# Kernel tuning notes

Hardware: AMD Instinct MI355X
Metric: run time of the kernel (lower is better)

## Reference

```python
import jax, jax.numpy as jnp
import numpy as np


def _procrustes_align(X, Y):
    """Batched similarity-transform (scipy-style Procrustes, reflection allowed).
    Aligns Y (pred) to X (target). X, Y: [B, N, 3]. Returns aligned Y: [B, N, 3].
    """
    muX = X.mean(axis=1, keepdims=True)                      # [B,1,3]
    muY = Y.mean(axis=1, keepdims=True)
    X0 = X - muX
    Y0 = Y - muY
    normX = jnp.sqrt((X0 ** 2).sum(axis=(1, 2), keepdims=True))  # [B,1,1]
    normY = jnp.sqrt((Y0 ** 2).sum(axis=(1, 2), keepdims=True))
    X0n = X0 / normX
    Y0n = Y0 / normY
    # 3x3 cross-covariance per batch element
    M = jnp.einsum('bni,bnj->bij', X0n, Y0n)                 # [B,3,3]
    U, s, Vt = jnp.linalg.svd(M)                             # batched tiny SVD
    # Optimal rotation Q = V @ U^T = (U @ Vt)^T  (minimizes ||Y0n @ Q - X0n||)
    Q = jnp.swapaxes(jnp.matmul(U, Vt), -1, -2)              # [B,3,3]
    traceTA = s.sum(-1)[:, None, None]                       # [B,1,1]
    Z = normX * traceTA * jnp.einsum('bni,bij->bnj', Y0n, Q) + muX
    return Z


def setup_inputs() -> dict:
    key = jax.random.key(0)
    k1, k2 = jax.random.split(key)
    B, N = 262144, 21
    pred_kp3d = jax.random.normal(k1, (B, N, 3), dtype=jnp.float32)
    target_kp3d = jax.random.normal(k2, (B, N, 3), dtype=jnp.float32)
    return {"pred_kp3d": pred_kp3d, "target_kp3d": target_kp3d}


def reference(pred_kp3d, target_kp3d):
    pred_aligned = _procrustes_align(target_kp3d, pred_kp3d)
    # mean per-joint Euclidean distance (PA-MPJPE style)
    err = jnp.sqrt(((pred_aligned - target_kp3d) ** 2).sum(-1)).mean()
    return err
```

## Files before the change

### kernel.cpp

```cpp
#include <hip/hip_runtime.h>
#include <math.h>

#define NPTS 21
#define FLB  63
#define BPW  32
#define THREADS 64
#define TVEC (BPW * FLB / 4)
#define FULLR (TVEC / 64)
#define TAILL (TVEC % 64)
#define KMAX 11

__device__ __forceinline__ void async_cp16(const float* g, float* l) {
    __builtin_amdgcn_global_load_lds(
        (__attribute__((address_space(1))) void*)g,
        (__attribute__((address_space(3))) void*)l,
        16, 0, 0);
}

__global__ __launch_bounds__(THREADS, 3)
void pa_mpjpe(const float* __restrict__ pred,
              const float* __restrict__ targ,
              float* __restrict__ ws,
              int B)
{
    __shared__ __align__(16) float ly[BPW * FLB];
    __shared__ __align__(16) float lx[BPW * FLB];

    const int lane = threadIdx.x & 63;
    const int b    = lane & (BPW - 1);
    const int sub  = (lane >> 5) & 1;
    const int b0   = blockIdx.x * BPW;

    {
        const float* gp = pred + (size_t)b0 * FLB;
        const float* gt = targ + (size_t)b0 * FLB;
        #pragma unroll
        for (int j = 0; j < FULLR; ++j)
            async_cp16(gp + 4 * (j * 64 + lane), ly + 4 * (j * 64));
        if (lane < TAILL)
            async_cp16(gp + 4 * (FULLR * 64 + lane), ly + 4 * (FULLR * 64));
        #pragma unroll
        for (int j = 0; j < FULLR; ++j)
            async_cp16(gt + 4 * (j * 64 + lane), lx + 4 * (j * 64));
        if (lane < TAILL)
            async_cp16(gt + 4 * (FULLR * 64 + lane), lx + 4 * (FULLR * 64));
    }
    __builtin_amdgcn_s_waitcnt(0x0F70);

    float py0[KMAX], py1[KMAX], py2[KMAX];
    float sy0=0.f, sy1=0.f, sy2=0.f, syy=0.f;
    float sx0=0.f, sx1=0.f, sx2=0.f;
    float m00=0,m01=0,m02=0, m10=0,m11=0,m12=0, m20=0,m21=0,m22=0;
    const int base = b * FLB;
    #pragma unroll
    for (int k = 0; k < KMAX; ++k) {
        const int n = 2 * k + sub;
        if (n < NPTS) {
            const int o = base + 3 * n;
            float a = ly[o+0], e = ly[o+1], c = ly[o+2];
            float u = lx[o+0], v = lx[o+1], x2 = lx[o+2];
            py0[k] = a; py1[k] = e; py2[k] = c;
            sy0 += a; sy1 += e; sy2 += c;
            syy = fmaf(a, a, fmaf(e, e, fmaf(c, c, syy)));
            sx0 += u; sx1 += v; sx2 += x2;
            m00 = fmaf(u,a,m00); m01 = fmaf(u,e,m01); m02 = fmaf(u,c,m02);
            m10 = fmaf(v,a,m10); m11 = fmaf(v,e,m11); m12 = fmaf(v,c,m12);
            m20 = fmaf(x2,a,m20); m21 = fmaf(x2,e,m21); m22 = fmaf(x2,c,m22);
        } else {
            py0[k] = 0.f; py1[k] = 0.f; py2[k] = 0.f;
        }
    }

    #define COMB(v) { v += __shfl_xor(v, 32, 64); }
    COMB(sy0) COMB(sy1) COMB(sy2) COMB(syy)
    COMB(sx0) COMB(sx1) COMB(sx2)
    COMB(m00) COMB(m01) COMB(m02)
    COMB(m10) COMB(m11) COMB(m12)
    COMB(m20) COMB(m21) COMB(m22)
    #undef COMB

    const float invN = 1.0f / (float)NPTS;
    float mux0 = sx0*invN, mux1 = sx1*invN, mux2 = sx2*invN;
    float muy0 = sy0*invN, muy1 = sy1*invN, muy2 = sy2*invN;
    float ny2  = syy - (sy0*sy0 + sy1*sy1 + sy2*sy2) * invN;
    float c00 = m00 - sx0*sy0*invN, c01 = m01 - sx0*sy1*invN, c02 = m02 - sx0*sy2*invN;
    float c10 = m10 - sx1*sy0*invN, c11 = m11 - sx1*sy1*invN, c12 = m12 - sx1*sy2*invN;
    float c20 = m20 - sx2*sy0*invN, c21 = m21 - sx2*sy1*invN, c22 = m22 - sx2*sy2*invN;

    float q00=c00, q01=c10, q02=c20,
          q10=c01, q11=c11, q12=c21,
          q20=c02, q21=c12, q22=c22;
    #pragma unroll
    for (int it = 0; it < 6; ++it) {
        float C00 = q11*q22 - q12*q21;
        float C01 = q12*q20 - q10*q22;
        float C02 = q10*q21 - q11*q20;
        float C10 = q02*q21 - q01*q22;
        float C11 = q00*q22 - q02*q20;
        float C12 = q01*q20 - q00*q21;
        float C20 = q01*q12 - q02*q11;
        float C21 = q02*q10 - q00*q12;
        float C22 = q00*q11 - q01*q10;
        float det = q00*C00 + q01*C01 + q02*C02;
        float ad  = fmaxf(fabsf(det), 1e-30f);
        float sdet = copysignf(ad, det);
        float g  = __expf(0.333333333f * __logf(ad));
        float ha = 0.5f / g;
        float hb = 0.5f * g / sdet;
        q00 = ha*q00 + hb*C00; q01 = ha*q01 + hb*C01; q02 = ha*q02 + hb*C02;
        q10 = ha*q10 + hb*C10; q11 = ha*q11 + hb*C11; q12 = ha*q12 + hb*C12;
        q20 = ha*q20 + hb*C20; q21 = ha*q21 + hb*C21; q22 = ha*q22 + hb*C22;
    }

    float trP = q00*c00 + q01*c10 + q02*c20
              + q10*c01 + q11*c11 + q12*c21
              + q20*c02 + q21*c12 + q22*c22;
    float kk = trP / ny2;
    float r00=kk*q00, r01=kk*q01, r02=kk*q02;
    float r10=kk*q10, r11=kk*q11, r12=kk*q12;
    float r20=kk*q20, r21=kk*q21, r22=kk*q22;

    float errsum = 0.0f;
    #pragma unroll
    for (int k = 0; k < KMAX; ++k) {
        const int n = 2 * k + sub;
        if (n < NPTS) {
            const int o = base + 3 * n;
            float xa = lx[o+0], xb = lx[o+1], xc = lx[o+2];
            float u = py0[k] - muy0, v = py1[k] - muy1, x2 = py2[k] - muy2;
            float z0 = fmaf(u, r00, fmaf(v, r10, fmaf(x2, r20, mux0))) - xa;
            float z1 = fmaf(u, r01, fmaf(v, r11, fmaf(x2, r21, mux1))) - xb;
            float z2 = fmaf(u, r02, fmaf(v, r12, fmaf(x2, r22, mux2))) - xc;
            errsum += sqrtf(fmaf(z0, z0, fmaf(z1, z1, z2*z2)));
        }
    }

    #pragma unroll
    for (int off = 32; off > 0; off >>= 1) errsum += __shfl_down(errsum, off, 64);
    if (lane == 0) ws[blockIdx.x] = errsum;
}

__global__ __launch_bounds__(256)
void pa_reduce(const float* __restrict__ ws, float* __restrict__ out,
               int nblk, float inv_total)
{
    __shared__ float sw[4];
    float s = 0.0f;
    const float4* w4 = (const float4*)ws;
    const int n4 = nblk >> 2;
    for (int i = threadIdx.x; i < n4; i += 256) {
        float4 v = w4[i];
        s += (v.x + v.y) + (v.z + v.w);
    }
    #pragma unroll
    for (int off = 32; off > 0; off >>= 1) s += __shfl_down(s, off, 64);
    if ((threadIdx.x & 63) == 0) sw[threadIdx.x >> 6] = s;
    __syncthreads();
    if (threadIdx.x == 0)
        out[0] = (sw[0] + sw[1] + sw[2] + sw[3]) * inv_total;
}

extern "C" void kernel_launch(void* const* d_in, const int* in_sizes, int n_in,
                              void* d_out, int out_size, void* d_ws, size_t ws_size,
                              hipStream_t stream)
{
    const float* pred = (const float*)d_in[0];
    const float* targ = (const float*)d_in[1];
    float* out = (float*)d_out;
    float* ws  = (float*)d_ws;

    int B = in_sizes[0] / FLB;
    int grid = (B + BPW - 1) / BPW;
    float inv_total = 1.0f / ((float)B * (float)NPTS);

    pa_mpjpe<<<grid, THREADS, 0, stream>>>(pred, targ, ws, B);
    pa_reduce<<<1, 256, 0, stream>>>(ws, out, grid, inv_total);
}
```

Baseline: 146.7 us.

## Make alignment kernel persistent with double-buffered async LDS staging

Replaces the one-block-per-chunk launch with a fixed grid of 1280 persistent single-wave blocks that stride over chunks of 32 batch elements. Each block double-buffers the pred and target tiles in LDS, issuing the async global-to-LDS loads for the next chunk while it computes the current one, so load latency overlaps with compute. This also cuts block launch overhead and shrinks the partial-sum array that the reduce kernel reads, which gains a scalar tail loop for counts not divisible by four. In exchange, LDS use per block doubles, which may reduce occupancy. The waitcnt encoding assumes a particular count of outstanding loads per chunk, and B is assumed to be a multiple of 32.

```diff
diff --git a/kernel.cpp b/kernel.cpp
--- a/kernel.cpp
+++ b/kernel.cpp
@@ -9,6 +9,7 @@
 #define FULLR (TVEC / 64)
 #define TAILL (TVEC % 64)
 #define KMAX 11
+#define GRID 1280
 
 __device__ __forceinline__ void async_cp16(const float* g, float* l) {
     __builtin_amdgcn_global_load_lds(
@@ -17,122 +18,150 @@
         16, 0, 0);
 }
 
+__device__ __forceinline__ void stage_chunk(const float* __restrict__ pred,
+                                            const float* __restrict__ targ,
+                                            int chunk, float* lyb, float* lxb,
+                                            int lane)
+{
+    const float* gp = pred + (size_t)chunk * (BPW * FLB);
+    const float* gt = targ + (size_t)chunk * (BPW * FLB);
+    #pragma unroll
+    for (int j = 0; j < FULLR; ++j)
+        async_cp16(gp + 4 * (j * 64 + lane), lyb + 4 * (j * 64));
+    if (lane < TAILL)
+        async_cp16(gp + 4 * (FULLR * 64 + lane), lyb + 4 * (FULLR * 64));
+    #pragma unroll
+    for (int j = 0; j < FULLR; ++j)
+        async_cp16(gt + 4 * (j * 64 + lane), lxb + 4 * (j * 64));
+    if (lane < TAILL)
+        async_cp16(gt + 4 * (FULLR * 64 + lane), lxb + 4 * (FULLR * 64));
+}
+
 __global__ __launch_bounds__(THREADS, 3)
 void pa_mpjpe(const float* __restrict__ pred,
               const float* __restrict__ targ,
               float* __restrict__ ws,
               int B)
 {
-    __shared__ __align__(16) float ly[BPW * FLB];
-    __shared__ __align__(16) float lx[BPW * FLB];
+    __shared__ __align__(16) float ly[2][BPW * FLB];
+    __shared__ __align__(16) float lx[2][BPW * FLB];
 
     const int lane = threadIdx.x & 63;
     const int b    = lane & (BPW - 1);
     const int sub  = (lane >> 5) & 1;
-    const int b0   = blockIdx.x * BPW;
-
-    {
-        const float* gp = pred + (size_t)b0 * FLB;
-        const float* gt = targ + (size_t)b0 * FLB;
+    const int base = b * FLB;
+    const int nch  = B / BPW;
+    const int stride = gridDim.x;
+
+    int c  = blockIdx.x;
+    stage_chunk(pred, targ, c, ly[0], lx[0], lane);
+    int nc = c + stride;
+    bool nif = (nc < nch);
+    if (nif) stage_chunk(pred, targ, nc, ly[1], lx[1], lane);
+
+    int cur = 0;
+    float errsum = 0.0f;
+
+    for (;;) {
+        if (nif) __builtin_amdgcn_s_waitcnt(0x4F70);
+        else     __builtin_amdgcn_s_waitcnt(0x0F70);
+        __builtin_amdgcn_sched_barrier(0);
+
+        const float* Y = ly[cur];
+        const float* X = lx[cur];
+
+        float py0[KMAX], py1[KMAX], py2[KMAX];
+        float sy0=0.f, sy1=0.f, sy2=0.f, syy=0.f;
+        float sx0=0.f, sx1=0.f, sx2=0.f;
+        float m00=0,m01=0,m02=0, m10=0,m11=0,m12=0, m20=0,m21=0,m22=0;
         #pragma unroll
-        for (int j = 0; j < FULLR; ++j)
-            async_cp16(gp + 4 * (j * 64 + lane), ly + 4 * (j * 64));
-        if (lane < TAILL)
-            async_cp16(gp + 4 * (FULLR * 64 + lane), ly + 4 * (FULLR * 64));
+        for (int k = 0; k < KMAX; ++k) {
+            const int n = 2 * k + sub;
+            if (n < NPTS) {
+                const int o = base + 3 * n;
+                float a = Y[o+0], e = Y[o+1], cc = Y[o+2];
+                float u = X[o+0], v = X[o+1], x2 = X[o+2];
+                py0[k] = a; py1[k] = e; py2[k] = cc;
+                sy0 += a; sy1 += e; sy2 += cc;
+                syy = fmaf(a, a, fmaf(e, e, fmaf(cc, cc, syy)));
+                sx0 += u; sx1 += v; sx2 += x2;
+                m00 = fmaf(u,a,m00); m01 = fmaf(u,e,m01); m02 = fmaf(u,cc,m02);
+                m10 = fmaf(v,a,m10); m11 = fmaf(v,e,m11); m12 = fmaf(v,cc,m12);
+                m20 = fmaf(x2,a,m20); m21 = fmaf(x2,e,m21); m22 = fmaf(x2,cc,m22);
+            } else {
+                py0[k] = 0.f; py1[k] = 0.f; py2[k] = 0.f;
+            }
+        }
+
+        #define COMB(v) { v += __shfl_xor(v, 32, 64); }
+        COMB(sy0) COMB(sy1) COMB(sy2) COMB(syy)
+        COMB(sx0) COMB(sx1) COMB(sx2)
+        COMB(m00) COMB(m01) COMB(m02)
+        COMB(m10) COMB(m11) COMB(m12)
+        COMB(m20) COMB(m21) COMB(m22)
+        #undef COMB
+
+        const float invN = 1.0f / (float)NPTS;
+        float mux0 = sx0*invN, mux1 = sx1*invN, mux2 = sx2*invN;
+        float muy0 = sy0*invN, muy1 = sy1*invN, muy2 = sy2*invN;
+        float ny2  = syy - (sy0*sy0 + sy1*sy1 + sy2*sy2) * invN;
+        float c00 = m00 - sx0*sy0*invN, c01 = m01 - sx0*sy1*invN, c02 = m02 - sx0*sy2*invN;
+        float c10 = m10 - sx1*sy0*invN, c11 = m11 - sx1*sy1*invN, c12 = m12 - sx1*sy2*invN;
+        float c20 = m20 - sx2*sy0*invN, c21 = m21 - sx2*sy1*invN, c22 = m22 - sx2*sy2*invN;
+
+        float q00=c00, q01=c10, q02=c20,
+              q10=c01, q11=c11, q12=c21,
+              q20=c02, q21=c12, q22=c22;
         #pragma unroll
-        for (int j = 0; j < FULLR; ++j)
-            async_cp16(gt + 4 * (j * 64 + lane), lx + 4 * (j * 64));
-        if (lane < TAILL)
-            async_cp16(gt + 4 * (FULLR * 64 + lane), lx + 4 * (FULLR * 64));
-    }
-    __builtin_amdgcn_s_waitcnt(0x0F70);
-
-    float py0[KMAX], py1[KMAX], py2[KMAX];
-    float sy0=0.f, sy1=0.f, sy2=0.f, syy=0.f;
-    float sx0=0.f, sx1=0.f, sx2=0.f;
-    float m00=0,m01=0,m02=0, m10=0,m11=0,m12=0, m20=0,m21=0,m22=0;
-    const int base = b * FLB;
-    #pragma unroll
-    for (int k = 0; k < KMAX; ++k) {
-        const int n = 2 * k + sub;
-        if (n < NPTS) {
-            const int o = base + 3 * n;
-            float a = ly[o+0], e = ly[o+1], c = ly[o+2];
-            float u = lx[o+0], v = lx[o+1], x2 = lx[o+2];
-            py0[k] = a; py1[k] = e; py2[k] = c;
-            sy0 += a; sy1 += e; sy2 += c;
-            syy = fmaf(a, a, fmaf(e, e, fmaf(c, c, syy)));
-            sx0 += u; sx1 += v; sx2 += x2;
-            m00 = fmaf(u,a,m00); m01 = fmaf(u,e,m01); m02 = fmaf(u,c,m02);
-            m10 = fmaf(v,a,m10); m11 = fmaf(v,e,m11); m12 = fmaf(v,c,m12);
-            m20 = fmaf(x2,a,m20); m21 = fmaf(x2,e,m21); m22 = fmaf(x2,c,m22);
-        } else {
-            py0[k] = 0.f; py1[k] = 0.f; py2[k] = 0.f;
+        for (int it = 0; it < 6; ++it) {
+            float C00 = q11*q22 - q12*q21;
+            float C01 = q12*q20 - q10*q22;
+            float C02 = q10*q21 - q11*q20;
+            float C10 = q02*q21 - q01*q22;
+            float C11 = q00*q22 - q02*q20;
+            float C12 = q01*q20 - q00*q21;
+            float C20 = q01*q12 - q02*q11;
+            float C21 = q02*q10 - q00*q12;
+            float C22 = q00*q11 - q01*q10;
+            float det = q00*C00 + q01*C01 + q02*C02;
+            float ad  = fmaxf(fabsf(det), 1e-30f);
+            float sdet = copysignf(ad, det);
+            float g  = __expf(0.333333333f * __logf(ad));
+            float ha = 0.5f / g;
+            float hb = 0.5f * g / sdet;
+            q00 = ha*q00 + hb*C00; q01 = ha*q01 + hb*C01; q02 = ha*q02 + hb*C02;
+            q10 = ha*q10 + hb*C10; q11 = ha*q11 + hb*C11; q12 = ha*q12 + hb*C12;
+            q20 = ha*q20 + hb*C20; q21 = ha*q21 + hb*C21; q22 = ha*q22 + hb*C22;
         }
-    }
-
-    #define COMB(v) { v += __shfl_xor(v, 32, 64); }
-    COMB(sy0) COMB(sy1) COMB(sy2) COMB(syy)
-    COMB(sx0) COMB(sx1) COMB(sx2)
-    COMB(m00) COMB(m01) COMB(m02)
-    COMB(m10) COMB(m11) COMB(m12)
-    COMB(m20) COMB(m21) COMB(m22)
-    #undef COMB
-
-    const float invN = 1.0f / (float)NPTS;
-    float mux0 = sx0*invN, mux1 = sx1*invN, mux2 = sx2*invN;
-    float muy0 = sy0*invN, muy1 = sy1*invN, muy2 = sy2*invN;
-    float ny2  = syy - (sy0*sy0 + sy1*sy1 + sy2*sy2) * invN;
-    float c00 = m00 - sx0*sy0*invN, c01 = m01 - sx0*sy1*invN, c02 = m02 - sx0*sy2*invN;
-    float c10 = m10 - sx1*sy0*invN, c11 = m11 - sx1*sy1*invN, c12 = m12 - sx1*sy2*invN;
-    float c20 = m20 - sx2*sy0*invN, c21 = m21 - sx2*sy1*invN, c22 = m22 - sx2*sy2*invN;
-
-    float q00=c00, q01=c10, q02=c20,
-          q10=c01, q11=c11, q12=c21,
-          q20=c02, q21=c12, q22=c22;
-    #pragma unroll
-    for (int it = 0; it < 6; ++it) {
-        float C00 = q11*q22 - q12*q21;
-        float C01 = q12*q20 - q10*q22;
-        float C02 = q10*q21 - q11*q20;
-        float C10 = q02*q21 - q01*q22;
-        float C11 = q00*q22 - q02*q20;
-        float C12 = q01*q20 - q00*q21;
-        float C20 = q01*q12 - q02*q11;
-        float C21 = q02*q10 - q00*q12;
-        float C22 = q00*q11 - q01*q10;
-        float det = q00*C00 + q01*C01 + q02*C02;
-        float ad  = fmaxf(fabsf(det), 1e-30f);
-        float sdet = copysignf(ad, det);
-        float g  = __expf(0.333333333f * __logf(ad));
-        float ha = 0.5f / g;
-        float hb = 0.5f * g / sdet;
-        q00 = ha*q00 + hb*C00; q01 = ha*q01 + hb*C01; q02 = ha*q02 + hb*C02;
-        q10 = ha*q10 + hb*C10; q11 = ha*q11 + hb*C11; q12 = ha*q12 + hb*C12;
-        q20 = ha*q20 + hb*C20; q21 = ha*q21 + hb*C21; q22 = ha*q22 + hb*C22;
-    }
-
-    float trP = q00*c00 + q01*c10 + q02*c20
-              + q10*c01 + q11*c11 + q12*c21
-              + q20*c02 + q21*c12 + q22*c22;
-    float kk = trP / ny2;
-    float r00=kk*q00, r01=kk*q01, r02=kk*q02;
-    float r10=kk*q10, r11=kk*q11, r12=kk*q12;
-    float r20=kk*q20, r21=kk*q21, r22=kk*q22;
-
-    float errsum = 0.0f;
-    #pragma unroll
-    for (int k = 0; k < KMAX; ++k) {
-        const int n = 2 * k + sub;
-        if (n < NPTS) {
-            const int o = base + 3 * n;
-            float xa = lx[o+0], xb = lx[o+1], xc = lx[o+2];
-            float u = py0[k] - muy0, v = py1[k] - muy1, x2 = py2[k] - muy2;
-            float z0 = fmaf(u, r00, fmaf(v, r10, fmaf(x2, r20, mux0))) - xa;
-            float z1 = fmaf(u, r01, fmaf(v, r11, fmaf(x2, r21, mux1))) - xb;
-            float z2 = fmaf(u, r02, fmaf(v, r12, fmaf(x2, r22, mux2))) - xc;
-            errsum += sqrtf(fmaf(z0, z0, fmaf(z1, z1, z2*z2)));
+
+        float trP = q00*c00 + q01*c10 + q02*c20
+                  + q10*c01 + q11*c11 + q12*c21
+                  + q20*c02 + q21*c12 + q22*c22;
+        float kk = trP / ny2;
+        float r00=kk*q00, r01=kk*q01, r02=kk*q02;
+        float r10=kk*q10, r11=kk*q11, r12=kk*q12;
+        float r20=kk*q20, r21=kk*q21, r22=kk*q22;
+
+        #pragma unroll
+        for (int k = 0; k < KMAX; ++k) {
+            const int n = 2 * k + sub;
+            if (n < NPTS) {
+                const int o = base + 3 * n;
+                float xa = X[o+0], xb = X[o+1], xc = X[o+2];
+                float u = py0[k] - muy0, v = py1[k] - muy1, x2 = py2[k] - muy2;
+                float z0 = fmaf(u, r00, fmaf(v, r10, fmaf(x2, r20, mux0))) - xa;
+                float z1 = fmaf(u, r01, fmaf(v, r11, fmaf(x2, r21, mux1))) - xb;
+                float z2 = fmaf(u, r02, fmaf(v, r12, fmaf(x2, r22, mux2))) - xc;
+                errsum += sqrtf(fmaf(z0, z0, fmaf(z1, z1, z2*z2)));
+            }
         }
+
+        if (!nif) break;
+        int pc = nc + stride;
+        bool pf = (pc < nch);
+        __builtin_amdgcn_sched_barrier(0);
+        if (pf) stage_chunk(pred, targ, pc, ly[cur], lx[cur], lane);
+        c = nc; nc = pc; nif = pf; cur ^= 1;
     }
 
     #pragma unroll
@@ -152,6 +181,7 @@
         float4 v = w4[i];
         s += (v.x + v.y) + (v.z + v.w);
     }
+    for (int i = 4 * n4 + threadIdx.x; i < nblk; i += 256) s += ws[i];
     #pragma unroll
     for (int off = 32; off > 0; off >>= 1) s += __shfl_down(s, off, 64);
     if ((threadIdx.x & 63) == 0) sw[threadIdx.x >> 6] = s;
@@ -170,7 +200,8 @@
     float* ws  = (float*)d_ws;
 
     int B = in_sizes[0] / FLB;
-    int grid = (B + BPW - 1) / BPW;
+    int nch = B / BPW;
+    int grid = (nch < GRID) ? nch : GRID;
     float inv_total = 1.0f / ((float)B * (float)NPTS);
 
     pa_mpjpe<<<grid, THREADS, 0, stream>>>(pred, targ, ws, B);
```

After: 164.4 us. +12.0%, slower.
